# Performance work log

Hardware: AMD Instinct MI355X
Metric: run time of the kernel (lower is better)

The kernel has to match this reference:

```python
import jax, jax.numpy as jnp
import numpy as np


def _structure_constants():
    # Octonion multiplication table: e_i * e_j = sum_k C[i,j,k] e_k.
    # e0 is the real unit; imaginary triples follow the standard Fano-plane
    # convention (Baez): e_a e_b = e_c for the cyclic triples below.
    C = np.zeros((8, 8, 8), dtype=np.float32)
    C[0, 0, 0] = 1.0
    for i in range(1, 8):
        C[0, i, i] = 1.0   # 1 * e_i = e_i
        C[i, 0, i] = 1.0   # e_i * 1 = e_i
        C[i, i, 0] = -1.0  # e_i * e_i = -1
    triples = [(1, 2, 3), (1, 4, 5), (1, 7, 6), (2, 4, 6), (2, 5, 7), (3, 4, 7), (3, 6, 5)]
    for (a, b, c) in triples:
        for (p, q, r) in ((a, b, c), (b, c, a), (c, a, b)):
            C[p, q, r] = 1.0
            C[q, p, r] = -1.0
    return C


_C = _structure_constants()

IN_FEATURES = 64
OUT_FEATURES = 64
BATCH = (16, 4096)


def setup_inputs() -> dict:
    key = jax.random.key(0)
    kx, kw, kb = jax.random.split(key, 3)
    x = jax.random.normal(kx, (*BATCH, IN_FEATURES, 8), dtype=jnp.float32)
    # 8 octonion-component weight matrices, stacked: [8, out, in]
    scale = 1.0 / np.sqrt(IN_FEATURES * 8)
    W = jax.random.normal(kw, (8, OUT_FEATURES, IN_FEATURES), dtype=jnp.float32) * scale
    b = jax.random.normal(kb, (OUT_FEATURES, 8), dtype=jnp.float32) * 0.01
    return {"x": x, "W": W, "b": b}


def reference(x, W, b):
    # out[..., o, k] = sum_{i,j,f} C[i,j,k] * W[i,o,f] * x[..., f, j] + b[o, k]
    # Fold the sparse structure constants into one block weight, then a single
    # contraction (the fused-GEMM formulation of the original 64-linear loop).
    C = jnp.asarray(_C, dtype=x.dtype)
    Wbig = jnp.einsum('iof,ijk->okfj', W, C)        # [out, 8, in, 8]
    out = jnp.einsum('...fj,okfj->...ok', x, Wbig)  # [..., out, 8]
    return out + b
```

## Files before the change

### kernel.cpp

```cpp
#include <hip/hip_runtime.h>
#include <hip/hip_bf16.h>

typedef __attribute__((ext_vector_type(8))) short short8;
typedef __attribute__((ext_vector_type(4))) float f32x4;
typedef __attribute__((address_space(1))) const unsigned int as1_u32;
typedef __attribute__((address_space(3))) unsigned int as3_u32;

#define BM 128
#define BN 128
#define BK 32
#define NKT 16

static __device__ __forceinline__ unsigned short f2bf(float f) {
    union { __hip_bfloat16 h; unsigned short u; } cv;
    cv.h = __float2bfloat16(f);
    return cv.u;
}

__device__ __forceinline__ void gload16(const void* g, void* l) {
    __builtin_amdgcn_global_load_lds((as1_u32*)g, (as3_u32*)l, 16, 0, 0);
}

__global__ __launch_bounds__(256) void build_wbig(const float* __restrict__ W,
                                                  unsigned short* __restrict__ WbigS) {
    __shared__ float C[8][8][8];
    const int t = threadIdx.x;
    for (int i = t; i < 512; i += 256) ((float*)C)[i] = 0.0f;
    __syncthreads();
    if (t == 0) {
        C[0][0][0] = 1.0f;
        for (int i = 1; i < 8; ++i) { C[0][i][i] = 1.0f; C[i][0][i] = 1.0f; C[i][i][0] = -1.0f; }
        const int tr[7][3] = {{1,2,3},{1,4,5},{1,7,6},{2,4,6},{2,5,7},{3,4,7},{3,6,5}};
        for (int q = 0; q < 7; ++q) {
            const int a = tr[q][0], b = tr[q][1], c = tr[q][2];
            const int p[3][3] = {{a,b,c},{b,c,a},{c,a,b}};
            for (int u = 0; u < 3; ++u) {
                C[p[u][0]][p[u][1]][p[u][2]] = 1.0f;
                C[p[u][1]][p[u][0]][p[u][2]] = -1.0f;
            }
        }
    }
    __syncthreads();
    const int e = blockIdx.x * 256 + t;
    const int m = e >> 9, kk = e & 511;
    const int o = m >> 3, k = m & 7, f = kk >> 3, j = kk & 7;
    float s = 0.0f;
#pragma unroll
    for (int i = 0; i < 8; ++i) s += C[i][j][k] * W[i * 4096 + o * 64 + f];

    const int nt = m >> 7, c = m & 127;
    const int H = kk >> 5, q = (kk >> 3) & 3, e8 = kk & 7;
    WbigS[((nt * 16 + H) * 4096) + c * 32 + ((q ^ (c & 3)) * 8) + e8] = f2bf(s);
}

__global__ __launch_bounds__(256, 3) void oct_gemm(const float* __restrict__ X,
                                                   const unsigned short* __restrict__ WbigS,
                                                   const float* __restrict__ Bias,
                                                   float* __restrict__ Out) {
    __shared__ float          Ah[2][4096];
    __shared__ unsigned short Bh[2][4096];

    const int bid = blockIdx.x;
    const int xcd = bid & 7;
    const int ix  = bid >> 3;
    const int mtile = xcd * 64 + (ix >> 2);
    const int nt    = ix & 3;
    const int rowBase = mtile * BM;
    const int colBase = nt * BN;

    const int t    = threadIdx.x;
    const int lane = t & 63;
    const int w    = t >> 6;
    const int wr   = w >> 1;
    const int wc   = w & 1;
    const int l15  = lane & 15;
    const int l4   = lane >> 4;

    const float* Asrc[4];
#pragma unroll
    for (int is = 0; is < 4; ++is) {
        const int s = (is * 4 + w) * 64 + lane;
        const int r = s >> 3, j = s & 7;
        const int c = (((j >> 1) ^ (r & 3)) << 3) + (((j & 1) ^ ((r >> 2) & 1)) << 2);
        Asrc[is] = X + (size_t)(rowBase + r) * 512 + c;
    }
    const unsigned short* Bsrc = WbigS + nt * (16 * 4096) + (size_t)w * 512 + lane * 8;

#define GLOAD(HB, H) do { _Pragma("unroll") \
    for (int is = 0; is < 4; ++is) \
        gload16(Asrc[is] + (H) * 32, &Ah[HB][(is * 4 + w) * 256]); \
    _Pragma("unroll") \
    for (int is = 0; is < 2; ++is) \
        gload16(Bsrc + (H) * 4096 + is * 2048, &Bh[HB][(is * 4 + w) * 512]); \
    } while (0)

    const int asub = (l15 >> 2) & 1;
    const int aoff = (wr * 64 + l15) * 32 + ((l4 ^ (l15 & 3)) << 3);
    const int boff = (wc * 64 + l15) * 32 + ((l4 ^ (l15 & 3)) << 3);

    f32x4 acc[4][4];
#pragma unroll
    for (int ni = 0; ni < 4; ++ni) {
        const float bv = Bias[colBase + wc * 64 + ni * 16 + l15];
#pragma unroll
        for (int mi = 0; mi < 4; ++mi) acc[mi][ni] = (f32x4){bv, bv, bv, bv};
    }

    GLOAD(0, 0);
    __syncthreads();

#pragma unroll
    for (int kt = 0; kt < NKT; ++kt) {
        if (kt + 1 < NKT) GLOAD((kt + 1) & 1, kt + 1);

        short8 bf[4];
#pragma unroll
        for (int ni = 0; ni < 4; ++ni)
            bf[ni] = *reinterpret_cast<const short8*>(&Bh[kt & 1][boff + ni * 512]);
#pragma unroll
        for (int mi = 0; mi < 4; ++mi) {
            const f32x4 lo = *reinterpret_cast<const f32x4*>(&Ah[kt & 1][aoff + mi * 512 + asub * 4]);
            const f32x4 hi = *reinterpret_cast<const f32x4*>(&Ah[kt & 1][aoff + mi * 512 + (asub ^ 1) * 4]);
            short8 af;
            af[0] = (short)f2bf(lo[0]); af[1] = (short)f2bf(lo[1]);
            af[2] = (short)f2bf(lo[2]); af[3] = (short)f2bf(lo[3]);
            af[4] = (short)f2bf(hi[0]); af[5] = (short)f2bf(hi[1]);
            af[6] = (short)f2bf(hi[2]); af[7] = (short)f2bf(hi[3]);
#pragma unroll
            for (int ni = 0; ni < 4; ++ni)
                acc[mi][ni] = __builtin_amdgcn_mfma_f32_16x16x32_bf16(af, bf[ni], acc[mi][ni], 0, 0, 0);
        }

        __syncthreads();
    }

#pragma unroll
    for (int mi = 0; mi < 4; ++mi) {
        const int row0 = rowBase + wr * 64 + mi * 16 + l4 * 4;
#pragma unroll
        for (int ni = 0; ni < 4; ++ni) {
            const int col = colBase + wc * 64 + ni * 16 + l15;
#pragma unroll
            for (int r = 0; r < 4; ++r)
                Out[(size_t)(row0 + r) * 512 + col] = acc[mi][ni][r];
        }
    }
#undef GLOAD
}

extern "C" void kernel_launch(void* const* d_in, const int* in_sizes, int n_in,
                              void* d_out, int out_size, void* d_ws, size_t ws_size,
                              hipStream_t stream) {
    const float* x = (const float*)d_in[0];
    const float* W = (const float*)d_in[1];
    const float* b = (const float*)d_in[2];
    float* out = (float*)d_out;
    unsigned short* WbigS = (unsigned short*)d_ws;

    build_wbig<<<1024, 256, 0, stream>>>(W, WbigS);
    oct_gemm<<<2048, 256, 0, stream>>>(x, WbigS, b, out);
}
```

Baseline: 78.52 us.

## Convert X to bf16 once into padded LDS with register prefetch, 512 threads

The A-tile path changes. X was streamed in fp32 via global_load_lds and converted to bf16 by every wave at each MFMA read. Now it is loaded into registers one k-tile ahead, converted once, and stored as bf16 into a padded LDS tile. BK doubles to 64 and the block grows to 8 waves, each computing a 64x32 sub-tile. This removes redundant conversions and halves LDS footprint for A. The cost is more register pressure, explicit VGPR staging of global loads, and half as many MFMAs per wave to hide latency.

```diff
diff --git a/kernel.cpp b/kernel.cpp
--- a/kernel.cpp
+++ b/kernel.cpp
@@ -8,8 +8,10 @@
 
 #define BM 128
 #define BN 128
-#define BK 32
-#define NKT 16
+#define BK 64
+#define NKT 8
+#define LDSTA 72
+#define A_ELE (128 * LDSTA)
 
 static __device__ __forceinline__ unsigned short f2bf(float f) {
     union { __hip_bfloat16 h; unsigned short u; } cv;
@@ -53,12 +55,12 @@
     WbigS[((nt * 16 + H) * 4096) + c * 32 + ((q ^ (c & 3)) * 8) + e8] = f2bf(s);
 }
 
-__global__ __launch_bounds__(256, 3) void oct_gemm(const float* __restrict__ X,
+__global__ __launch_bounds__(512, 4) void oct_gemm(const float* __restrict__ X,
                                                    const unsigned short* __restrict__ WbigS,
                                                    const float* __restrict__ Bias,
                                                    float* __restrict__ Out) {
-    __shared__ float          Ah[2][4096];
-    __shared__ unsigned short Bh[2][4096];
+    __shared__ unsigned short As[2][A_ELE];
+    __shared__ unsigned short Bs[2][2][4096];
 
     const int bid = blockIdx.x;
     const int xcd = bid & 7;
@@ -71,66 +73,84 @@
     const int t    = threadIdx.x;
     const int lane = t & 63;
     const int w    = t >> 6;
-    const int wr   = w >> 1;
-    const int wc   = w & 1;
+    const int wr   = w >> 2;
+    const int wc   = w & 3;
     const int l15  = lane & 15;
     const int l4   = lane >> 4;
 
-    const float* Asrc[4];
-#pragma unroll
-    for (int is = 0; is < 4; ++is) {
-        const int s = (is * 4 + w) * 64 + lane;
-        const int r = s >> 3, j = s & 7;
-        const int c = (((j >> 1) ^ (r & 3)) << 3) + (((j & 1) ^ ((r >> 2) & 1)) << 2);
-        Asrc[is] = X + (size_t)(rowBase + r) * 512 + c;
-    }
-    const unsigned short* Bsrc = WbigS + nt * (16 * 4096) + (size_t)w * 512 + lane * 8;
+    const int srow = t >> 2;
+    const int scol = (t & 3) * 16;
+    const float* Xp = X + (size_t)(rowBase + srow) * 512 + scol;
 
-#define GLOAD(HB, H) do { _Pragma("unroll") \
-    for (int is = 0; is < 4; ++is) \
-        gload16(Asrc[is] + (H) * 32, &Ah[HB][(is * 4 + w) * 256]); \
-    _Pragma("unroll") \
-    for (int is = 0; is < 2; ++is) \
-        gload16(Bsrc + (H) * 4096 + is * 2048, &Bh[HB][(is * 4 + w) * 512]); \
+    const unsigned short* Bsrc = WbigS + nt * (16 * 4096) + t * 8;
+
+    f32x4 va[4];
+
+#define ISSUE_A(KT) do { _Pragma("unroll") \
+    for (int l = 0; l < 4; ++l) \
+        va[l] = *reinterpret_cast<const f32x4*>(Xp + (KT) * BK + l * 4); \
     } while (0)
 
-    const int asub = (l15 >> 2) & 1;
-    const int aoff = (wr * 64 + l15) * 32 + ((l4 ^ (l15 & 3)) << 3);
-    const int boff = (wc * 64 + l15) * 32 + ((l4 ^ (l15 & 3)) << 3);
+#define GLOAD_B(BUF, KT) do { _Pragma("unroll") \
+    for (int kk = 0; kk < 2; ++kk) \
+        gload16(Bsrc + (2 * (KT) + kk) * 4096, &Bs[BUF][kk][w * 512]); \
+    } while (0)
 
-    f32x4 acc[4][4];
+#define WRITE_A(BUF) do { \
+    short8 p0, p1; \
+    p0[0]=(short)f2bf(va[0][0]); p0[1]=(short)f2bf(va[0][1]); \
+    p0[2]=(short)f2bf(va[0][2]); p0[3]=(short)f2bf(va[0][3]); \
+    p0[4]=(short)f2bf(va[1][0]); p0[5]=(short)f2bf(va[1][1]); \
+    p0[6]=(short)f2bf(va[1][2]); p0[7]=(short)f2bf(va[1][3]); \
+    p1[0]=(short)f2bf(va[2][0]); p1[1]=(short)f2bf(va[2][1]); \
+    p1[2]=(short)f2bf(va[2][2]); p1[3]=(short)f2bf(va[2][3]); \
+    p1[4]=(short)f2bf(va[3][0]); p1[5]=(short)f2bf(va[3][1]); \
+    p1[6]=(short)f2bf(va[3][2]); p1[7]=(short)f2bf(va[3][3]); \
+    *reinterpret_cast<short8*>(&As[BUF][srow * LDSTA + scol]) = p0; \
+    *reinterpret_cast<short8*>(&As[BUF][srow * LDSTA + scol + 8]) = p1; \
+    } while (0)
+
+    f32x4 acc[4][2];
 #pragma unroll
-    for (int ni = 0; ni < 4; ++ni) {
-        const float bv = Bias[colBase + wc * 64 + ni * 16 + l15];
+    for (int ni = 0; ni < 2; ++ni) {
+        const float bv = Bias[colBase + wc * 32 + ni * 16 + l15];
 #pragma unroll
         for (int mi = 0; mi < 4; ++mi) acc[mi][ni] = (f32x4){bv, bv, bv, bv};
     }
 
-    GLOAD(0, 0);
+    ISSUE_A(0);
+    GLOAD_B(0, 0);
+    WRITE_A(0);
     __syncthreads();
 
 #pragma unroll
     for (int kt = 0; kt < NKT; ++kt) {
-        if (kt + 1 < NKT) GLOAD((kt + 1) & 1, kt + 1);
-
-        short8 bf[4];
-#pragma unroll
-        for (int ni = 0; ni < 4; ++ni)
-            bf[ni] = *reinterpret_cast<const short8*>(&Bh[kt & 1][boff + ni * 512]);
-#pragma unroll
-        for (int mi = 0; mi < 4; ++mi) {
-            const f32x4 lo = *reinterpret_cast<const f32x4*>(&Ah[kt & 1][aoff + mi * 512 + asub * 4]);
-            const f32x4 hi = *reinterpret_cast<const f32x4*>(&Ah[kt & 1][aoff + mi * 512 + (asub ^ 1) * 4]);
-            short8 af;
-            af[0] = (short)f2bf(lo[0]); af[1] = (short)f2bf(lo[1]);
-            af[2] = (short)f2bf(lo[2]); af[3] = (short)f2bf(lo[3]);
-            af[4] = (short)f2bf(hi[0]); af[5] = (short)f2bf(hi[1]);
-            af[6] = (short)f2bf(hi[2]); af[7] = (short)f2bf(hi[3]);
-#pragma unroll
-            for (int ni = 0; ni < 4; ++ni)
-                acc[mi][ni] = __builtin_amdgcn_mfma_f32_16x16x32_bf16(af, bf[ni], acc[mi][ni], 0, 0, 0);
+        if (kt + 1 < NKT) {
+            ISSUE_A(kt + 1);
+            GLOAD_B((kt + 1) & 1, kt + 1);
         }
 
+#pragma unroll
+        for (int kk = 0; kk < 2; ++kk) {
+            short8 b[2];
+#pragma unroll
+            for (int ni = 0; ni < 2; ++ni) {
+                const int c = wc * 32 + ni * 16 + l15;
+                b[ni] = *reinterpret_cast<const short8*>(
+                    &Bs[kt & 1][kk][c * 32 + ((l4 ^ (l15 & 3)) << 3)]);
+            }
+#pragma unroll
+            for (int mi = 0; mi < 4; ++mi) {
+                const short8 a = *reinterpret_cast<const short8*>(
+                    &As[kt & 1][(wr * 64 + mi * 16 + l15) * LDSTA + kk * 32 + l4 * 8]);
+#pragma unroll
+                for (int ni = 0; ni < 2; ++ni)
+                    acc[mi][ni] = __builtin_amdgcn_mfma_f32_16x16x32_bf16(
+                        a, b[ni], acc[mi][ni], 0, 0, 0);
+            }
+        }
+
+        if (kt + 1 < NKT) WRITE_A((kt + 1) & 1);
         __syncthreads();
     }
 
@@ -138,14 +158,16 @@
     for (int mi = 0; mi < 4; ++mi) {
         const int row0 = rowBase + wr * 64 + mi * 16 + l4 * 4;
 #pragma unroll
-        for (int ni = 0; ni < 4; ++ni) {
-            const int col = colBase + wc * 64 + ni * 16 + l15;
+        for (int ni = 0; ni < 2; ++ni) {
+            const int col = colBase + wc * 32 + ni * 16 + l15;
 #pragma unroll
             for (int r = 0; r < 4; ++r)
                 Out[(size_t)(row0 + r) * 512 + col] = acc[mi][ni][r];
         }
     }
-#undef GLOAD
+#undef ISSUE_A
+#undef GLOAD_B
+#undef WRITE_A
 }
 
 extern "C" void kernel_launch(void* const* d_in, const int* in_sizes, int n_in,
@@ -158,5 +180,5 @@
     unsigned short* WbigS = (unsigned short*)d_ws;
 
     build_wbig<<<1024, 256, 0, stream>>>(W, WbigS);
-    oct_gemm<<<2048, 256, 0, stream>>>(x, WbigS, b, out);
+    oct_gemm<<<2048, 512, 0, stream>>>(x, WbigS, b, out);
 }
```

New measurement: 83.30 us. +6.1%, slower.
